# Optimization experiments

Measured on AMD Instinct MI355X. Metric: run time of the kernel, lower is better.

Reference implementation:

```python
import jax, jax.numpy as jnp
import numpy as np

B, S, H, D = 2, 2048, 16, 64
HID = H * D
NEG_INF = -10000.0

def setup_inputs() -> dict:
    key = jax.random.key(0)
    ks = jax.random.split(key, 4)
    std = 0.02
    return {
        'x': jax.random.normal(ks[0], (B, S, HID), dtype=jnp.float32),
        'mask': jnp.ones((B, S), dtype=jnp.int32),
        'Wq': jax.random.normal(ks[1], (HID, HID), dtype=jnp.float32) * std,
        'bq': jnp.zeros((HID,), dtype=jnp.float32),
        'Wk': jax.random.normal(ks[2], (HID, HID), dtype=jnp.float32) * std,
        'bk': jnp.zeros((HID,), dtype=jnp.float32),
        'Wv': jax.random.normal(ks[3], (HID, HID), dtype=jnp.float32) * std,
        'bv': jnp.zeros((HID,), dtype=jnp.float32),
    }

def reference(x, mask, Wq, bq, Wk, bk, Wv, bv):
    b, s, _ = x.shape
    def split_heads(t):  # [b,s,HID] -> [b,H,s,D]
        return t.reshape(b, s, H, D).transpose(0, 2, 1, 3)
    q = split_heads(x @ Wq + bq)
    k = split_heads(x @ Wk + bk)
    v = split_heads(x @ Wv + bv)
    scores = jnp.einsum('bhqd,bhkd->bhqk', q, k) / jnp.sqrt(jnp.float32(D))
    # additive padding mask: [b,1,1,s] broadcast over query positions and heads
    adder = (1.0 - mask.astype(scores.dtype))[:, None, None, :] * NEG_INF
    probs = jax.nn.softmax(scores + adder, axis=-1)
    ctx = jnp.einsum('bhqk,bhkd->bhqd', probs, v)  # [b,H,s,D]
    return ctx.transpose(0, 2, 1, 3).reshape(b, s, HID)
```

## Files before the change

kernel.cpp:

```cpp
#include <hip/hip_runtime.h>
#include <cstddef>

constexpr int Bc = 2, Sc = 2048, Hc = 16, Dc = 64, HIDc = 1024;
#define NEG_INF -10000.0f

typedef _Float16 half8  __attribute__((ext_vector_type(8)));
typedef _Float16 half4  __attribute__((ext_vector_type(4)));
typedef float   floatx4 __attribute__((ext_vector_type(4)));

__global__ __launch_bounds__(256) void cvt_x_kernel(const float* __restrict__ x,
                                                    _Float16* __restrict__ xh) {
    int i = (blockIdx.x * 256 + threadIdx.x) * 8;
    float4 a = *(const float4*)(x + i);
    float4 b = *(const float4*)(x + i + 4);
    half8 h;
    h[0] = (_Float16)a.x; h[1] = (_Float16)a.y; h[2] = (_Float16)a.z; h[3] = (_Float16)a.w;
    h[4] = (_Float16)b.x; h[5] = (_Float16)b.y; h[6] = (_Float16)b.z; h[7] = (_Float16)b.w;
    *(half8*)(xh + i) = h;
}

__global__ __launch_bounds__(256) void cvt_w_kernel(const float* __restrict__ Wq,
                                                    const float* __restrict__ Wk,
                                                    const float* __restrict__ Wv,
                                                    _Float16* __restrict__ Wt) {
    const float* W = (blockIdx.z == 0) ? Wq : (blockIdx.z == 1) ? Wk : Wv;
    _Float16* out = Wt + (size_t)blockIdx.z * HIDc * HIDc;
    __shared__ _Float16 T[64][65];
    const int t = threadIdx.x;
    const int kb = blockIdx.x * 64, nb = blockIdx.y * 64;
    const int r = t >> 2, c4 = (t & 3) * 16;
    #pragma unroll
    for (int i = 0; i < 16; i += 4) {
        float4 a = *(const float4*)(W + (size_t)(kb + r) * HIDc + nb + c4 + i);
        T[c4 + i + 0][r] = (_Float16)a.x;
        T[c4 + i + 1][r] = (_Float16)a.y;
        T[c4 + i + 2][r] = (_Float16)a.z;
        T[c4 + i + 3][r] = (_Float16)a.w;
    }
    __syncthreads();
    const int n = t >> 2, k4 = (t & 3) * 16;
    half8 o0, o1;
    #pragma unroll
    for (int j = 0; j < 8; ++j) { o0[j] = T[n][k4 + j]; o1[j] = T[n][k4 + 8 + j]; }
    *(half8*)(out + (size_t)(nb + n) * HIDc + kb + k4)     = o0;
    *(half8*)(out + (size_t)(nb + n) * HIDc + kb + k4 + 8) = o1;
}

#define PSTR 40
__global__ __launch_bounds__(256, 2) void proj_kernel(
    const _Float16* __restrict__ xh, const _Float16* __restrict__ Wt,
    const float* __restrict__ bq, const float* __restrict__ bk, const float* __restrict__ bv,
    _Float16* __restrict__ qw, _Float16* __restrict__ kw, _Float16* __restrict__ vt)
{
    const int z = blockIdx.z;
    const _Float16* Wz = Wt + (size_t)z * HIDc * HIDc;
    const float* bias = (z == 0) ? bq : (z == 1) ? bk : bv;

    __shared__ _Float16 As[2][128 * PSTR];
    __shared__ _Float16 Bs[2][128 * PSTR];

    const int t = threadIdx.x;
    const int lane = t & 63, w = t >> 6;
    const int quad = lane >> 4, l16 = lane & 15;
    const int m0 = blockIdx.y * 128, n0 = blockIdx.x * 128;
    const int wm = (w >> 1) * 64, wn = (w & 1) * 64;
    const int sr = t >> 1, sh = (t & 1) * 16;

    floatx4 acc[4][4];
    #pragma unroll
    for (int mb = 0; mb < 4; ++mb)
        #pragma unroll
        for (int nb = 0; nb < 4; ++nb) acc[mb][nb] = floatx4{0.f, 0.f, 0.f, 0.f};

    {
        const _Float16* ap = xh + (size_t)(m0 + sr) * HIDc + sh;
        const _Float16* bp = Wz + (size_t)(n0 + sr) * HIDc + sh;
        *(uint4*)(As[0] + sr * PSTR + sh)     = *(const uint4*)(ap);
        *(uint4*)(As[0] + sr * PSTR + sh + 8) = *(const uint4*)(ap + 8);
        *(uint4*)(Bs[0] + sr * PSTR + sh)     = *(const uint4*)(bp);
        *(uint4*)(Bs[0] + sr * PSTR + sh + 8) = *(const uint4*)(bp + 8);
    }
    __syncthreads();

    #pragma unroll 2
    for (int it = 0; it < HIDc / 32; ++it) {
        const int cur = it & 1;
        const int kn = (it + 1 < HIDc / 32) ? (it + 1) * 32 : 0;
        const _Float16* ap = xh + (size_t)(m0 + sr) * HIDc + kn + sh;
        const _Float16* bp = Wz + (size_t)(n0 + sr) * HIDc + kn + sh;
        uint4 a0 = *(const uint4*)(ap);
        uint4 a1 = *(const uint4*)(ap + 8);
        uint4 b0 = *(const uint4*)(bp);
        uint4 b1 = *(const uint4*)(bp + 8);

        half8 af[4], bf[4];
        #pragma unroll
        for (int mb = 0; mb < 4; ++mb)
            af[mb] = *(const half8*)(As[cur] + (wm + mb * 16 + l16) * PSTR + quad * 8);
        #pragma unroll
        for (int nb = 0; nb < 4; ++nb)
            bf[nb] = *(const half8*)(Bs[cur] + (wn + nb * 16 + l16) * PSTR + quad * 8);
        #pragma unroll
        for (int mb = 0; mb < 4; ++mb)
            #pragma unroll
            for (int nb = 0; nb < 4; ++nb)
                acc[mb][nb] = __builtin_amdgcn_mfma_f32_16x16x32_f16(
                    af[mb], bf[nb], acc[mb][nb], 0, 0, 0);

        *(uint4*)(As[cur ^ 1] + sr * PSTR + sh)     = a0;
        *(uint4*)(As[cur ^ 1] + sr * PSTR + sh + 8) = a1;
        *(uint4*)(Bs[cur ^ 1] + sr * PSTR + sh)     = b0;
        *(uint4*)(Bs[cur ^ 1] + sr * PSTR + sh + 8) = b1;
        __syncthreads();
    }

    #pragma unroll
    for (int nb = 0; nb < 4; ++nb) {
        const int N = n0 + wn + nb * 16 + l16;
        const float bi = bias[N];
        const int h = N >> 6, d = N & 63;
        #pragma unroll
        for (int mb = 0; mb < 4; ++mb) {
            #pragma unroll
            for (int r = 0; r < 4; ++r) {
                const int M = m0 + wm + mb * 16 + quad * 4 + r;
                const int bI = M >> 11, s = M & (Sc - 1);
                const float v = acc[mb][nb][r] + bi;
                if (z == 0)
                    qw[(((size_t)(bI * Hc + h)) * Sc + s) * Dc + d] = (_Float16)(v * 0.125f);
                else if (z == 1)
                    kw[(((size_t)(bI * Hc + h)) * Sc + s) * Dc + d] = (_Float16)v;
                else
                    vt[(((size_t)(bI * Hc + h)) * Dc + d) * Sc + s] = (_Float16)v;
            }
        }
    }
}

__global__ __launch_bounds__(256, 2) void attn_kernel(
    const _Float16* __restrict__ qw, const _Float16* __restrict__ kw,
    const _Float16* __restrict__ vt, const int* __restrict__ mask,
    float* __restrict__ out)
{
    __shared__ float adder[Sc];
    __shared__ __align__(16) _Float16 Ks[2][64][72];
    __shared__ __align__(16) _Float16 Vs[2][64][72];

    const int t = threadIdx.x;
    const int lane = t & 63, w = t >> 6;
    const int quad = lane >> 4, l16 = lane & 15;
    const int bh = blockIdx.y;
    const int bI = bh >> 4, h = bh & 15;

    const _Float16* Qp = qw + (size_t)bh * Sc * Dc;
    const _Float16* Kp = kw + (size_t)bh * Sc * Dc;
    const _Float16* Vp = vt + (size_t)bh * Dc * Sc;

    const int srow = t >> 3;
    const int scol = (t & 7) * 8;

    {
        const int4* mp = (const int4*)(mask + bI * Sc);
        #pragma unroll
        for (int i = 0; i < 2; ++i) {
            int4 m4 = mp[t * 2 + i];
            int base = (t * 2 + i) * 4;
            adder[base + 0] = (1.0f - (float)m4.x) * NEG_INF;
            adder[base + 1] = (1.0f - (float)m4.y) * NEG_INF;
            adder[base + 2] = (1.0f - (float)m4.z) * NEG_INF;
            adder[base + 3] = (1.0f - (float)m4.w) * NEG_INF;
        }
    }
    #pragma unroll
    for (int hf = 0; hf < 2; ++hf) {
        const int row = srow + 32 * hf;
        uint4 kv = *(const uint4*)(Kp + (size_t)row * Dc + scol);
        uint4 vv = *(const uint4*)(Vp + (size_t)row * Sc + scol);
        *(uint4*)(&Ks[0][row][scol]) = kv;
        *(uint4*)(&Vs[0][row][scol]) = vv;
    }

    const int qrow = blockIdx.x * 128 + w * 32;
    half8 aq[2][2];
    #pragma unroll
    for (int s = 0; s < 2; ++s)
        #pragma unroll
        for (int hh = 0; hh < 2; ++hh)
            aq[s][hh] = *(const half8*)(Qp + (size_t)(qrow + 16 * s + l16) * Dc
                                        + hh * 32 + quad * 8);

    floatx4 o[2][4];
    #pragma unroll
    for (int s = 0; s < 2; ++s)
        #pragma unroll
        for (int db = 0; db < 4; ++db) o[s][db] = floatx4{0.f, 0.f, 0.f, 0.f};
    float lsum[2] = {0.f, 0.f};

    __syncthreads();

    #pragma unroll 2
    for (int it = 0; it < Sc / 64; ++it) {
        const int cur = it & 1;
        const int kt = it * 64;
        const int ktn = (it + 1 < Sc / 64) ? kt + 64 : 0;
        uint4 kstg[2], vstg[2];
        #pragma unroll
        for (int hf = 0; hf < 2; ++hf) {
            const int row = srow + 32 * hf;
            kstg[hf] = *(const uint4*)(Kp + (size_t)(ktn + row) * Dc + scol);
            vstg[hf] = *(const uint4*)(Vp + (size_t)row * Sc + ktn + scol);
        }

        half8 kb[4][2];
        half4 vb[4][4];
        #pragma unroll
        for (int nb = 0; nb < 4; ++nb)
            #pragma unroll
            for (int hh = 0; hh < 2; ++hh)
                kb[nb][hh] = *(const half8*)(&Ks[cur][nb * 16 + l16][hh * 32 + quad * 8]);
        #pragma unroll
        for (int nb = 0; nb < 4; ++nb)
            #pragma unroll
            for (int db = 0; db < 4; ++db)
                vb[nb][db] = *(const half4*)(&Vs[cur][db * 16 + l16][nb * 16 + quad * 4]);

        floatx4 st[2][4];
        #pragma unroll
        for (int s = 0; s < 2; ++s)
            #pragma unroll
            for (int nb = 0; nb < 4; ++nb) {
                floatx4 acc = floatx4{0.f, 0.f, 0.f, 0.f};
                acc = __builtin_amdgcn_mfma_f32_16x16x32_f16(kb[nb][0], aq[s][0], acc, 0, 0, 0);
                acc = __builtin_amdgcn_mfma_f32_16x16x32_f16(kb[nb][1], aq[s][1], acc, 0, 0, 0);
                st[s][nb] = acc;
            }

        half4 pa[2][4];
        #pragma unroll
        for (int nb = 0; nb < 4; ++nb) {
            const float4 a4 = *(const float4*)&adder[kt + nb * 16 + quad * 4];
            const float ad[4] = {a4.x, a4.y, a4.z, a4.w};
            #pragma unroll
            for (int s = 0; s < 2; ++s)
                #pragma unroll
                for (int r = 0; r < 4; ++r) {
                    const float p = __expf(st[s][nb][r] + ad[r]);
                    lsum[s] += p;
                    pa[s][nb][r] = (_Float16)p;
                }
        }

        #pragma unroll
        for (int s = 0; s < 2; ++s)
            #pragma unroll
            for (int nb = 0; nb < 4; ++nb)
                #pragma unroll
                for (int db = 0; db < 4; ++db)
                    o[s][db] = __builtin_amdgcn_mfma_f32_16x16x16f16(
                        pa[s][nb], vb[nb][db], o[s][db], 0, 0, 0);

        #pragma unroll
        for (int hf = 0; hf < 2; ++hf) {
            const int row = srow + 32 * hf;
            *(uint4*)(&Ks[cur ^ 1][row][scol]) = kstg[hf];
            *(uint4*)(&Vs[cur ^ 1][row][scol]) = vstg[hf];
        }
        __syncthreads();
    }

    #pragma unroll
    for (int s = 0; s < 2; ++s) {
        lsum[s] += __shfl_xor(lsum[s], 16, 64);
        lsum[s] += __shfl_xor(lsum[s], 32, 64);
    }
    float* op = out + (size_t)bI * Sc * HIDc + h * Dc;
    #pragma unroll
    for (int s = 0; s < 2; ++s)
        #pragma unroll
        for (int r = 0; r < 4; ++r) {
            const float inv = 1.0f / __shfl(lsum[s], quad * 4 + r, 64);
            const int q = qrow + 16 * s + quad * 4 + r;
            #pragma unroll
            for (int db = 0; db < 4; ++db)
                op[(size_t)q * HIDc + db * 16 + l16] = o[s][db][r] * inv;
        }
}

extern "C" void kernel_launch(void* const* d_in, const int* in_sizes, int n_in,
                              void* d_out, int out_size, void* d_ws, size_t ws_size,
                              hipStream_t stream) {
    const float* x    = (const float*)d_in[0];
    const int*   mask = (const int*)  d_in[1];
    const float* Wq   = (const float*)d_in[2];
    const float* bq   = (const float*)d_in[3];
    const float* Wk   = (const float*)d_in[4];
    const float* bk   = (const float*)d_in[5];
    const float* Wv   = (const float*)d_in[6];
    const float* bv   = (const float*)d_in[7];
    float* out = (float*)d_out;

    char* ws = (char*)d_ws;
    _Float16* xh = (_Float16*)(ws);
    _Float16* Wt = (_Float16*)(ws + (size_t)8  * 1024 * 1024);
    _Float16* qw = (_Float16*)(ws + (size_t)14 * 1024 * 1024);
    _Float16* kw = (_Float16*)(ws + (size_t)22 * 1024 * 1024);
    _Float16* vt = (_Float16*)(ws + (size_t)30 * 1024 * 1024);

    cvt_x_kernel<<<(Bc * Sc * HIDc) / (256 * 8), 256, 0, stream>>>(x, xh);
    cvt_w_kernel<<<dim3(HIDc / 64, HIDc / 64, 3), 256, 0, stream>>>(Wq, Wk, Wv, Wt);
    proj_kernel<<<dim3(HIDc / 128, (Bc * Sc) / 128, 3), 256, 0, stream>>>(
        xh, Wt, bq, bk, bv, qw, kw, vt);
    attn_kernel<<<dim3(Sc / 128, Bc * Hc), 256, 0, stream>>>(qw, kw, vt, mask, out);
}
```

Measured before the change: 189.9 us.

## Fold mask into MFMA accumulator, use exp2, MFMA row sums, coalesce V stores

The attention kernel now pre-scales Q by log2e and uses exp2. It seeds the QK MFMA accumulator with the mask adder, removing the separate add. Row sums come from an extra MFMA against a ones vector instead of scalar adds and shuffles. V tiles are stored in a permuted LDS layout so each lane reads half8 instead of half4, and s_setprio brackets the MFMA phases. The projection kernel transposes V through shared memory so vt is written with coalesced 16-byte stores. The cost is extra MFMA work for the sums and more complex indexing.

```diff
diff --git a/kernel.cpp b/kernel.cpp
--- a/kernel.cpp
+++ b/kernel.cpp
@@ -3,6 +3,7 @@
 
 constexpr int Bc = 2, Sc = 2048, Hc = 16, Dc = 64, HIDc = 1024;
 #define NEG_INF -10000.0f
+#define LOG2E 1.44269504088896340736f
 
 typedef _Float16 half8  __attribute__((ext_vector_type(8)));
 typedef _Float16 half4  __attribute__((ext_vector_type(4)));
@@ -56,8 +57,7 @@
     const _Float16* Wz = Wt + (size_t)z * HIDc * HIDc;
     const float* bias = (z == 0) ? bq : (z == 1) ? bk : bv;
 
-    __shared__ _Float16 As[2][128 * PSTR];
-    __shared__ _Float16 Bs[2][128 * PSTR];
+    __shared__ __align__(16) _Float16 SM[4][128 * PSTR];
 
     const int t = threadIdx.x;
     const int lane = t & 63, w = t >> 6;
@@ -75,10 +75,10 @@
     {
         const _Float16* ap = xh + (size_t)(m0 + sr) * HIDc + sh;
         const _Float16* bp = Wz + (size_t)(n0 + sr) * HIDc + sh;
-        *(uint4*)(As[0] + sr * PSTR + sh)     = *(const uint4*)(ap);
-        *(uint4*)(As[0] + sr * PSTR + sh + 8) = *(const uint4*)(ap + 8);
-        *(uint4*)(Bs[0] + sr * PSTR + sh)     = *(const uint4*)(bp);
-        *(uint4*)(Bs[0] + sr * PSTR + sh + 8) = *(const uint4*)(bp + 8);
+        *(uint4*)(SM[0] + sr * PSTR + sh)     = *(const uint4*)(ap);
+        *(uint4*)(SM[0] + sr * PSTR + sh + 8) = *(const uint4*)(ap + 8);
+        *(uint4*)(SM[2] + sr * PSTR + sh)     = *(const uint4*)(bp);
+        *(uint4*)(SM[2] + sr * PSTR + sh + 8) = *(const uint4*)(bp + 8);
     }
     __syncthreads();
 
@@ -96,10 +96,10 @@
         half8 af[4], bf[4];
         #pragma unroll
         for (int mb = 0; mb < 4; ++mb)
-            af[mb] = *(const half8*)(As[cur] + (wm + mb * 16 + l16) * PSTR + quad * 8);
+            af[mb] = *(const half8*)(SM[cur] + (wm + mb * 16 + l16) * PSTR + quad * 8);
         #pragma unroll
         for (int nb = 0; nb < 4; ++nb)
-            bf[nb] = *(const half8*)(Bs[cur] + (wn + nb * 16 + l16) * PSTR + quad * 8);
+            bf[nb] = *(const half8*)(SM[2 + cur] + (wn + nb * 16 + l16) * PSTR + quad * 8);
         #pragma unroll
         for (int mb = 0; mb < 4; ++mb)
             #pragma unroll
@@ -107,13 +107,42 @@
                 acc[mb][nb] = __builtin_amdgcn_mfma_f32_16x16x32_f16(
                     af[mb], bf[nb], acc[mb][nb], 0, 0, 0);
 
-        *(uint4*)(As[cur ^ 1] + sr * PSTR + sh)     = a0;
-        *(uint4*)(As[cur ^ 1] + sr * PSTR + sh + 8) = a1;
-        *(uint4*)(Bs[cur ^ 1] + sr * PSTR + sh)     = b0;
-        *(uint4*)(Bs[cur ^ 1] + sr * PSTR + sh + 8) = b1;
+        *(uint4*)(SM[cur ^ 1] + sr * PSTR + sh)           = a0;
+        *(uint4*)(SM[cur ^ 1] + sr * PSTR + sh + 8)       = a1;
+        *(uint4*)(SM[2 + (cur ^ 1)] + sr * PSTR + sh)     = b0;
+        *(uint4*)(SM[2 + (cur ^ 1)] + sr * PSTR + sh + 8) = b1;
         __syncthreads();
     }
 
+    if (z == 2) {
+        _Float16* T = &SM[0][0];
+        #pragma unroll
+        for (int nb = 0; nb < 4; ++nb) {
+            const int n = wn + nb * 16 + l16;
+            const float bi = bias[n0 + n];
+            #pragma unroll
+            for (int mb = 0; mb < 4; ++mb) {
+                half4 h4;
+                #pragma unroll
+                for (int r = 0; r < 4; ++r) h4[r] = (_Float16)(acc[mb][nb][r] + bi);
+                *(half4*)(T + n * 136 + wm + mb * 16 + quad * 4) = h4;
+            }
+        }
+        __syncthreads();
+        const int bI0 = m0 >> 11, m0s = m0 & (Sc - 1);
+        #pragma unroll
+        for (int p = 0; p < 2; ++p) {
+            const int n = p * 64 + (t >> 2);
+            const int N = n0 + n, hh = N >> 6, d = N & 63;
+            _Float16* vrow = vt + (((size_t)(bI0 * Hc + hh)) * Dc + d) * Sc + m0s;
+            #pragma unroll
+            for (int j = 0; j < 4; ++j) {
+                const int c = (t & 3) * 32 + j * 8;
+                *(uint4*)(vrow + c) = *(const uint4*)(T + n * 136 + c);
+            }
+        }
+        return;
+    }
     #pragma unroll
     for (int nb = 0; nb < 4; ++nb) {
         const int N = n0 + wn + nb * 16 + l16;
@@ -127,11 +156,10 @@
                 const int bI = M >> 11, s = M & (Sc - 1);
                 const float v = acc[mb][nb][r] + bi;
                 if (z == 0)
-                    qw[(((size_t)(bI * Hc + h)) * Sc + s) * Dc + d] = (_Float16)(v * 0.125f);
-                else if (z == 1)
+                    qw[(((size_t)(bI * Hc + h)) * Sc + s) * Dc + d] =
+                        (_Float16)(v * (0.125f * LOG2E));
+                else
                     kw[(((size_t)(bI * Hc + h)) * Sc + s) * Dc + d] = (_Float16)v;
-                else
-                    vt[(((size_t)(bI * Hc + h)) * Dc + d) * Sc + s] = (_Float16)v;
             }
         }
     }
@@ -142,7 +170,7 @@
     const _Float16* __restrict__ vt, const int* __restrict__ mask,
     float* __restrict__ out)
 {
-    __shared__ float adder[Sc];
+    __shared__ __align__(16) float adder[Sc];
     __shared__ __align__(16) _Float16 Ks[2][64][72];
     __shared__ __align__(16) _Float16 Vs[2][64][72];
 
@@ -158,6 +186,8 @@
 
     const int srow = t >> 3;
     const int scol = (t & 7) * 8;
+    const int m7 = t & 7;
+    const int vc0 = 32 * (m7 & 1) + 4 * (m7 >> 1);
 
     {
         const int4* mp = (const int4*)(mask + bI * Sc);
@@ -165,10 +195,10 @@
         for (int i = 0; i < 2; ++i) {
             int4 m4 = mp[t * 2 + i];
             int base = (t * 2 + i) * 4;
-            adder[base + 0] = (1.0f - (float)m4.x) * NEG_INF;
-            adder[base + 1] = (1.0f - (float)m4.y) * NEG_INF;
-            adder[base + 2] = (1.0f - (float)m4.z) * NEG_INF;
-            adder[base + 3] = (1.0f - (float)m4.w) * NEG_INF;
+            adder[base + 0] = (1.0f - (float)m4.x) * (NEG_INF * LOG2E);
+            adder[base + 1] = (1.0f - (float)m4.y) * (NEG_INF * LOG2E);
+            adder[base + 2] = (1.0f - (float)m4.z) * (NEG_INF * LOG2E);
+            adder[base + 3] = (1.0f - (float)m4.w) * (NEG_INF * LOG2E);
         }
     }
     #pragma unroll
@@ -177,7 +207,8 @@
         uint4 kv = *(const uint4*)(Kp + (size_t)row * Dc + scol);
         uint4 vv = *(const uint4*)(Vp + (size_t)row * Sc + scol);
         *(uint4*)(&Ks[0][row][scol]) = kv;
-        *(uint4*)(&Vs[0][row][scol]) = vv;
+        *(uint2*)(&Vs[0][row][vc0])      = make_uint2(vv.x, vv.y);
+        *(uint2*)(&Vs[0][row][vc0 + 16]) = make_uint2(vv.z, vv.w);
     }
 
     const int qrow = blockIdx.x * 128 + w * 32;
@@ -189,12 +220,14 @@
             aq[s][hh] = *(const half8*)(Qp + (size_t)(qrow + 16 * s + l16) * Dc
                                         + hh * 32 + quad * 8);
 
-    floatx4 o[2][4];
-    #pragma unroll
-    for (int s = 0; s < 2; ++s)
+    floatx4 o[2][4], osum[2];
+    #pragma unroll
+    for (int s = 0; s < 2; ++s) {
+        osum[s] = floatx4{0.f, 0.f, 0.f, 0.f};
         #pragma unroll
         for (int db = 0; db < 4; ++db) o[s][db] = floatx4{0.f, 0.f, 0.f, 0.f};
-    float lsum[2] = {0.f, 0.f};
+    }
+    const half4 ones4 = {(_Float16)1.f, (_Float16)1.f, (_Float16)1.f, (_Float16)1.f};
 
     __syncthreads();
 
@@ -212,73 +245,74 @@
         }
 
         half8 kb[4][2];
-        half4 vb[4][4];
         #pragma unroll
         for (int nb = 0; nb < 4; ++nb)
             #pragma unroll
             for (int hh = 0; hh < 2; ++hh)
                 kb[nb][hh] = *(const half8*)(&Ks[cur][nb * 16 + l16][hh * 32 + quad * 8]);
-        #pragma unroll
-        for (int nb = 0; nb < 4; ++nb)
-            #pragma unroll
-            for (int db = 0; db < 4; ++db)
-                vb[nb][db] = *(const half4*)(&Vs[cur][db * 16 + l16][nb * 16 + quad * 4]);
+
+        half4 vb[4][4];
+        #pragma unroll
+        for (int db = 0; db < 4; ++db)
+            #pragma unroll
+            for (int hf2 = 0; hf2 < 2; ++hf2) {
+                const half8 v8 = *(const half8*)(&Vs[cur][db * 16 + l16][quad * 16 + hf2 * 8]);
+                vb[hf2 * 2 + 0][db] = __builtin_shufflevector(v8, v8, 0, 1, 2, 3);
+                vb[hf2 * 2 + 1][db] = __builtin_shufflevector(v8, v8, 4, 5, 6, 7);
+            }
 
         floatx4 st[2][4];
+        __builtin_amdgcn_s_setprio(1);
+        #pragma unroll
+        for (int nb = 0; nb < 4; ++nb) {
+            const floatx4 adv = *(const floatx4*)(&adder[kt + nb * 16 + quad * 4]);
+            #pragma unroll
+            for (int s = 0; s < 2; ++s) {
+                floatx4 x0 = __builtin_amdgcn_mfma_f32_16x16x32_f16(kb[nb][0], aq[s][0], adv, 0, 0, 0);
+                st[s][nb]  = __builtin_amdgcn_mfma_f32_16x16x32_f16(kb[nb][1], aq[s][1], x0, 0, 0, 0);
+            }
+        }
+        __builtin_amdgcn_s_setprio(0);
+
+        half4 pa[2][4];
         #pragma unroll
         for (int s = 0; s < 2; ++s)
             #pragma unroll
+            for (int nb = 0; nb < 4; ++nb)
+                #pragma unroll
+                for (int r = 0; r < 4; ++r)
+                    pa[s][nb][r] = (_Float16)__builtin_amdgcn_exp2f(st[s][nb][r]);
+
+        __builtin_amdgcn_s_setprio(1);
+        #pragma unroll
+        for (int s = 0; s < 2; ++s)
+            #pragma unroll
             for (int nb = 0; nb < 4; ++nb) {
-                floatx4 acc = floatx4{0.f, 0.f, 0.f, 0.f};
-                acc = __builtin_amdgcn_mfma_f32_16x16x32_f16(kb[nb][0], aq[s][0], acc, 0, 0, 0);
-                acc = __builtin_amdgcn_mfma_f32_16x16x32_f16(kb[nb][1], aq[s][1], acc, 0, 0, 0);
-                st[s][nb] = acc;
-            }
-
-        half4 pa[2][4];
-        #pragma unroll
-        for (int nb = 0; nb < 4; ++nb) {
-            const float4 a4 = *(const float4*)&adder[kt + nb * 16 + quad * 4];
-            const float ad[4] = {a4.x, a4.y, a4.z, a4.w};
-            #pragma unroll
-            for (int s = 0; s < 2; ++s)
-                #pragma unroll
-                for (int r = 0; r < 4; ++r) {
-                    const float p = __expf(st[s][nb][r] + ad[r]);
-                    lsum[s] += p;
-                    pa[s][nb][r] = (_Float16)p;
-                }
-        }
-
-        #pragma unroll
-        for (int s = 0; s < 2; ++s)
-            #pragma unroll
-            for (int nb = 0; nb < 4; ++nb)
+                osum[s] = __builtin_amdgcn_mfma_f32_16x16x16f16(pa[s][nb], ones4, osum[s], 0, 0, 0);
                 #pragma unroll
                 for (int db = 0; db < 4; ++db)
                     o[s][db] = __builtin_amdgcn_mfma_f32_16x16x16f16(
                         pa[s][nb], vb[nb][db], o[s][db], 0, 0, 0);
+            }
+        __builtin_amdgcn_s_setprio(0);
 
         #pragma unroll
         for (int hf = 0; hf < 2; ++hf) {
             const int row = srow + 32 * hf;
             *(uint4*)(&Ks[cur ^ 1][row][scol]) = kstg[hf];
-            *(uint4*)(&Vs[cur ^ 1][row][scol]) = vstg[hf];
+            const uint4 vv = vstg[hf];
+            *(uint2*)(&Vs[cur ^ 1][row][vc0])      = make_uint2(vv.x, vv.y);
+            *(uint2*)(&Vs[cur ^ 1][row][vc0 + 16]) = make_uint2(vv.z, vv.w);
         }
         __syncthreads();
     }
 
-    #pragma unroll
-    for (int s = 0; s < 2; ++s) {
-        lsum[s] += __shfl_xor(lsum[s], 16, 64);
-        lsum[s] += __shfl_xor(lsum[s], 32, 64);
-    }
     float* op = out + (size_t)bI * Sc * HIDc + h * Dc;
     #pragma unroll
     for (int s = 0; s < 2; ++s)
         #pragma unroll
         for (int r = 0; r < 4; ++r) {
-            const float inv = 1.0f / __shfl(lsum[s], quad * 4 + r, 64);
+            const float inv = __builtin_amdgcn_rcpf(osum[s][r]);
             const int q = qrow + 16 * s + quad * 4 + r;
             #pragma unroll
             for (int db = 0; db < 4; ++db)
```

Measured after the change: 179.2 us. 1.06x faster.
